# Performance work log

Hardware: AMD Instinct MI355X
Metric: run time of the kernel (lower is better)

The kernel has to match this reference:

```python
import jax, jax.numpy as jnp
import numpy as np

N, E, F_IN = 50000, 800000, 64
H, C1, C2 = 4, 32, 64
NUM_GRAPHS, NUM_CLASSES = 128, 8
NEG_SLOPE = 0.2


def _glorot(key, shape):
    fan_in, fan_out = shape[1], shape[0]
    lim = (6.0 / (fan_in + fan_out)) ** 0.5
    return jax.random.uniform(key, shape, jnp.float32, -lim, lim)


def setup_inputs() -> dict:
    key = jax.random.key(0)
    ks = jax.random.split(key, 20)
    x = jax.random.normal(ks[0], (N, F_IN), jnp.float32)
    edge_index = jax.random.randint(ks[1], (2, E), 0, N, jnp.int64)
    batch = jnp.sort(jax.random.randint(ks[2], (N,), 0, NUM_GRAPHS, jnp.int64))
    d1, d2 = H * C1, H * C2
    return {
        "x": x, "edge_index": edge_index, "batch": batch,
        # GATv2 layer 1 (F_IN -> 32, 4 heads)
        "Wl1": _glorot(ks[3], (d1, F_IN)), "bl1": jnp.zeros((d1,), jnp.float32),
        "Wr1": _glorot(ks[4], (d1, F_IN)), "br1": jnp.zeros((d1,), jnp.float32),
        "att1": _glorot(ks[5], (H, C1)), "bias1": jnp.zeros((d1,), jnp.float32),
        # GATv2 layer 2 (128 -> 64, 4 heads)
        "Wl2": _glorot(ks[6], (d2, d1)), "bl2": jnp.zeros((d2,), jnp.float32),
        "Wr2": _glorot(ks[7], (d2, d1)), "br2": jnp.zeros((d2,), jnp.float32),
        "att2": _glorot(ks[8], (H, C2)), "bias2": jnp.zeros((d2,), jnp.float32),
        # classifier: Linear(256,128) -> ReLU -> (Dropout eval=id) -> Linear(128,8)
        "Wf1": _glorot(ks[9], (128, d2)), "bf1": jnp.zeros((128,), jnp.float32),
        "Wf2": _glorot(ks[10], (NUM_CLASSES, 128)), "bf2": jnp.zeros((NUM_CLASSES,), jnp.float32),
    }


def _gatv2(x, src, dst, Wl, bl, Wr, br, att, bias, heads, out_ch):
    # PyG GATv2Conv: xl = lin_l(x) (source), xr = lin_r(x) (target)
    xl = (x @ Wl.T + bl).reshape(N, heads, out_ch)
    xr = (x @ Wr.T + br).reshape(N, heads, out_ch)
    # per-edge score: att . LeakyReLU(xl[j] + xr[i])  -> [E', H]
    e = jnp.sum(jax.nn.leaky_relu(xl[src] + xr[dst], NEG_SLOPE) * att, axis=-1)
    # destination-grouped softmax (self-loops guarantee every node has an edge)
    emax = jax.ops.segment_max(e, dst, num_segments=N)
    ex = jnp.exp(e - emax[dst])
    denom = jax.ops.segment_sum(ex, dst, num_segments=N)
    alpha = ex / denom[dst]  # [E', H]
    out = jax.ops.segment_sum(alpha[:, :, None] * xl[src], dst, num_segments=N)
    return out.reshape(N, heads * out_ch) + bias


def reference(x, edge_index, batch, Wl1, bl1, Wr1, br1, att1, bias1,
              Wl2, bl2, Wr2, br2, att2, bias2, Wf1, bf1, Wf2, bf2):
    # add self loops (PyG default add_self_loops=True)
    loops = jnp.arange(N, dtype=edge_index.dtype)
    src = jnp.concatenate([edge_index[0], loops])
    dst = jnp.concatenate([edge_index[1], loops])
    h = jax.nn.elu(_gatv2(x, src, dst, Wl1, bl1, Wr1, br1, att1, bias1, H, C1))
    h = jax.nn.elu(_gatv2(h, src, dst, Wl2, bl2, Wr2, br2, att2, bias2, H, C2))
    # global mean pool over graphs
    sums = jax.ops.segment_sum(h, batch, num_segments=NUM_GRAPHS)
    cnts = jax.ops.segment_sum(jnp.ones((N,), h.dtype), batch, num_segments=NUM_GRAPHS)
    pooled = sums / jnp.maximum(cnts, 1.0)[:, None]  # [G, 256]
    # classifier (dropout inactive at inference)
    z = jax.nn.relu(pooled @ Wf1.T + bf1)
    return z @ Wf2.T + bf2
```

## Files before the change

kernel.cpp:

```cpp
#include <hip/hip_runtime.h>
#include <hip/hip_bf16.h>
#include <math.h>

#define NN 50000
#define NE 800000
#define NEP (NE + NN)
#define NG 128
#define PSPLIT 16

typedef unsigned short u16;
typedef __bf16 bf16x8 __attribute__((ext_vector_type(8)));
typedef float f32x4 __attribute__((ext_vector_type(4)));

__device__ __forceinline__ float lrelu02(float v) {
  return fmaxf(v, 0.0f) + 0.2f * fminf(v, 0.0f);
}
__device__ __forceinline__ float eluf(float v) {
  return v > 0.0f ? v : expm1f(v);
}
__device__ __forceinline__ float bflo(unsigned u) {
  union { unsigned i; float f; } c; c.i = u << 16; return c.f;
}
__device__ __forceinline__ float bfhi(unsigned u) {
  union { unsigned i; float f; } c; c.i = u & 0xffff0000u; return c.f;
}
__device__ __forceinline__ bf16x8 load8(const u16* p) {
  union { uint4 u; bf16x8 v; } c;
  c.u = *(const uint4*)p;
  return c.v;
}

__global__ __launch_bounds__(256) void k_deg(const int* __restrict__ ei, int* __restrict__ deg) {
  int t = blockIdx.x * 256 + threadIdx.x;
  if (t >= NEP) return;
  int dst = (t < NE) ? ei[NE + t] : (t - NE);
  atomicAdd(&deg[dst], 1);
}

__global__ __launch_bounds__(1024) void k_scan(const int* __restrict__ deg, int* __restrict__ rowptr) {
  __shared__ int part[1024];
  int t = threadIdx.x;
  const int CH = (NN + 1023) >> 10;
  int b = t * CH;
  int e = min(b + CH, NN);
  int s = 0;
  for (int i = b; i < e; ++i) s += deg[i];
  part[t] = s;
  __syncthreads();
  for (int off = 1; off < 1024; off <<= 1) {
    int v = (t >= off) ? part[t - off] : 0;
    __syncthreads();
    part[t] += v;
    __syncthreads();
  }
  int run = (t == 0) ? 0 : part[t - 1];
  for (int i = b; i < e; ++i) { rowptr[i] = run; run += deg[i]; }
  if (t == 1023) rowptr[NN] = part[1023];
}

__global__ __launch_bounds__(256) void k_scatter(const int* __restrict__ ei, const int* __restrict__ rowptr,
                                                 int* __restrict__ fill, int* __restrict__ srcidx) {
  int t = blockIdx.x * 256 + threadIdx.x;
  if (t >= NEP) return;
  int src, dst;
  if (t < NE) { src = ei[t]; dst = ei[NE + t]; } else { src = t - NE; dst = src; }
  int pos = atomicAdd(&fill[dst], 1);
  srcidx[rowptr[dst] + pos] = src;
}

__global__ __launch_bounds__(256) void k_cvtx(const float* __restrict__ x, u16* __restrict__ o, int n4) {
  int t = blockIdx.x * 256 + threadIdx.x;
  if (t >= n4) return;
  float4 v = ((const float4*)x)[t];
  __hip_bfloat16 b[4] = {__float2bfloat16(v.x), __float2bfloat16(v.y),
                         __float2bfloat16(v.z), __float2bfloat16(v.w)};
  ((uint2*)o)[t] = *(uint2*)b;
}

__global__ __launch_bounds__(256) void k_cvtw(const float* __restrict__ w1, const float* __restrict__ w2,
                                              const float* __restrict__ w3, const float* __restrict__ w4,
                                              u16* __restrict__ o) {
  int t = blockIdx.x * 256 + threadIdx.x;
  if (t >= 81920) return;
  float v;
  if (t < 8192) v = w1[t];
  else if (t < 16384) v = w2[t - 8192];
  else if (t < 49152) v = w3[t - 16384];
  else v = w4[t - 49152];
  __hip_bfloat16 b = __float2bfloat16(v);
  o[t] = *(u16*)&b;
}

template <int K>
__global__ __launch_bounds__(256) void k_mfma(const u16* __restrict__ Xb,
                                              const u16* __restrict__ Wlb, const u16* __restrict__ Wrb,
                                              const float* __restrict__ bl, const float* __restrict__ br,
                                              __hip_bfloat16* __restrict__ Yl, float* __restrict__ Yr,
                                              int dout) {
  int lane = threadIdx.x & 63;
  int wid = threadIdx.x >> 6;
  int r0 = blockIdx.x * 64 + wid * 16;
  int c0 = blockIdx.y * 64;
  bool isR = (blockIdx.z != 0);
  const u16* W = isR ? Wrb : Wlb;
  const float* bias = isR ? br : bl;

  int arow = min(r0 + (lane & 15), NN - 1);
  int koff = (lane >> 4) * 8;
  const u16* ap = Xb + (size_t)arow * K + koff;
  const u16* bp = W + (size_t)(c0 + (lane & 15)) * K + koff;

  f32x4 acc[4] = {};
#pragma unroll
  for (int ks = 0; ks < K / 32; ++ks) {
    bf16x8 a  = load8(ap + ks * 32);
    bf16x8 b0 = load8(bp + ks * 32);
    bf16x8 b1 = load8(bp + 16 * K + ks * 32);
    bf16x8 b2 = load8(bp + 32 * K + ks * 32);
    bf16x8 b3 = load8(bp + 48 * K + ks * 32);
    acc[0] = __builtin_amdgcn_mfma_f32_16x16x32_bf16(a, b0, acc[0], 0, 0, 0);
    acc[1] = __builtin_amdgcn_mfma_f32_16x16x32_bf16(a, b1, acc[1], 0, 0, 0);
    acc[2] = __builtin_amdgcn_mfma_f32_16x16x32_bf16(a, b2, acc[2], 0, 0, 0);
    acc[3] = __builtin_amdgcn_mfma_f32_16x16x32_bf16(a, b3, acc[3], 0, 0, 0);
  }

  int orow = r0 + ((lane >> 4) << 2);
  int ocol = c0 + (lane & 15);
#pragma unroll
  for (int t = 0; t < 4; ++t) {
    int col = ocol + t * 16;
    float bv = bias[col];
    if (!isR) {
#pragma unroll
      for (int v = 0; v < 4; ++v) {
        int row = orow + v;
        if (row < NN) Yl[(size_t)row * dout + col] = __float2bfloat16(acc[t][v] + bv);
      }
    } else {
#pragma unroll
      for (int v = 0; v < 4; ++v) {
        int row = orow + v;
        if (row < NN) Yr[(size_t)row * dout + col] = acc[t][v] + bv;
      }
    }
  }
}

template <int D, bool OBF16>
__global__ __launch_bounds__(256) void k_fused(const int* __restrict__ rowptr, const int* __restrict__ srcidx,
                                               const __hip_bfloat16* __restrict__ xl, const float* __restrict__ xr,
                                               const float* __restrict__ att, const float* __restrict__ bias,
                                               void* __restrict__ outv) {
  constexpr int V = D / 64;
  int lane = threadIdx.x & 63;
  int node = blockIdx.x * 4 + (threadIdx.x >> 6);
  if (node >= NN) return;
  int lo = rowptr[node], hi = rowptr[node + 1];

  float xrv[V], attv[V];
#pragma unroll
  for (int q = 0; q < V; ++q) {
    xrv[q]  = xr[(size_t)node * D + lane * V + q];
    attv[q] = att[lane * V + q];
  }

  const unsigned* xl1 = (const unsigned*)xl;
  const uint2*    xl2 = (const uint2*)xl;

  float denom = 0.f;
  float acc[V] = {};

  auto gather = [&](int j, float* xv) {
    if constexpr (V == 2) {
      unsigned u = xl1[(size_t)j * (D / 2) + lane];
      xv[0] = bflo(u); xv[1] = bfhi(u);
    } else {
      uint2 u = xl2[(size_t)j * (D / 4) + lane];
      xv[0] = bflo(u.x); xv[1] = bfhi(u.x);
      xv[2] = bflo(u.y); xv[3] = bfhi(u.y);
    }
  };
  auto score_partial = [&](const float* xv) {
    float p = 0.f;
#pragma unroll
    for (int q = 0; q < V; ++q) p += attv[q] * lrelu02(xv[q] + xrv[q]);
    return p;
  };
  auto update = [&](float sh, const float* xv) {
    float w = __expf(sh);
    denom += w;
#pragma unroll
    for (int q = 0; q < V; ++q) acc[q] += w * xv[q];
  };

  int s = lo;
  for (; s + 3 < hi; s += 4) {
    int j0 = srcidx[s], j1 = srcidx[s + 1], j2 = srcidx[s + 2], j3 = srcidx[s + 3];
    float xv0[V], xv1[V], xv2[V], xv3[V];
    gather(j0, xv0); gather(j1, xv1); gather(j2, xv2); gather(j3, xv3);
    float p0 = score_partial(xv0);
    float p1 = score_partial(xv1);
    float p2 = score_partial(xv2);
    float p3 = score_partial(xv3);
#pragma unroll
    for (int off = 1; off < 16; off <<= 1) {
      p0 += __shfl_xor(p0, off);
      p1 += __shfl_xor(p1, off);
      p2 += __shfl_xor(p2, off);
      p3 += __shfl_xor(p3, off);
    }
    update(p0, xv0); update(p1, xv1); update(p2, xv2); update(p3, xv3);
  }
  for (; s < hi; ++s) {
    int j0 = srcidx[s];
    float xv0[V];
    gather(j0, xv0);
    float p0 = score_partial(xv0);
#pragma unroll
    for (int off = 1; off < 16; off <<= 1) p0 += __shfl_xor(p0, off);
    update(p0, xv0);
  }

  float rd = 1.0f / denom;
  float vals[V];
#pragma unroll
  for (int q = 0; q < V; ++q) vals[q] = eluf(acc[q] * rd + bias[lane * V + q]);

  if constexpr (OBF16) {
    __hip_bfloat16 tmp[V];
#pragma unroll
    for (int q = 0; q < V; ++q) tmp[q] = __float2bfloat16(vals[q]);
    if constexpr (V == 2) ((unsigned*)outv)[(size_t)node * (D / 2) + lane] = *(unsigned*)tmp;
    else                  ((uint2*)outv)[(size_t)node * (D / 4) + lane] = *(uint2*)tmp;
  } else {
    float* out = (float*)outv;
#pragma unroll
    for (int q = 0; q < V; ++q) out[(size_t)node * D + lane * V + q] = vals[q];
  }
}

__device__ __forceinline__ int lowerb(const int* __restrict__ a, int n, int v) {
  int lo = 0, hi = n;
  while (lo < hi) { int mid = (lo + hi) >> 1; if (a[mid] < v) lo = mid + 1; else hi = mid; }
  return lo;
}

__global__ __launch_bounds__(256) void k_pool(const float* __restrict__ h2, const int* __restrict__ batch,
                                              float* __restrict__ pooled_p) {
  int g = blockIdx.x, sp = blockIdx.y, t = threadIdx.x;
  __shared__ int sh[2];
  if (t < 2) sh[t] = lowerb(batch, NN, g + t);
  __syncthreads();
  int lo = sh[0], hi = sh[1];
  int cnt = hi - lo;
  int chunk = (cnt + PSPLIT - 1) / PSPLIT;
  int b = lo + sp * chunk;
  int e = min(b + chunk, hi);
  float acc = 0.f;
  for (int n = b; n < e; ++n) acc += h2[(size_t)n * 256 + t];
  pooled_p[((size_t)g * PSPLIT + sp) * 256 + t] = acc;
}

__global__ __launch_bounds__(128) void k_cls(const float* __restrict__ pooled_p, const int* __restrict__ batch,
                                             const float* __restrict__ Wf1, const float* __restrict__ bf1,
                                             const float* __restrict__ Wf2, const float* __restrict__ bf2,
                                             float* __restrict__ out) {
  __shared__ float p[256];
  __shared__ float z[128];
  __shared__ int sh[2];
  int g = blockIdx.x, t = threadIdx.x;
  if (t < 2) sh[t] = lowerb(batch, NN, g + t);
  __syncthreads();
  float cnt = (float)(sh[1] - sh[0]);
  float rinv = 1.0f / fmaxf(cnt, 1.0f);
  const float* pp = pooled_p + (size_t)g * PSPLIT * 256;
#pragma unroll 1
  for (int c = t; c < 256; c += 128) {
    float s = 0.f;
#pragma unroll
    for (int sp = 0; sp < PSPLIT; ++sp) s += pp[sp * 256 + c];
    p[c] = s * rinv;
  }
  __syncthreads();
  float a = bf1[t];
  const float* wr = Wf1 + (size_t)t * 256;
  for (int k = 0; k < 256; ++k) a += p[k] * wr[k];
  z[t] = fmaxf(a, 0.f);
  __syncthreads();
  if (t < 8) {
    float o = bf2[t];
    const float* w2 = Wf2 + t * 128;
    for (int k = 0; k < 128; ++k) o += z[k] * w2[k];
    out[g * 8 + t] = o;
  }
}

extern "C" void kernel_launch(void* const* d_in, const int* in_sizes, int n_in,
                              void* d_out, int out_size, void* d_ws, size_t ws_size,
                              hipStream_t stream) {
  const float* x     = (const float*)d_in[0];
  const int*   ei    = (const int*)d_in[1];
  const int*   batch = (const int*)d_in[2];
  const float* Wl1 = (const float*)d_in[3];
  const float* bl1 = (const float*)d_in[4];
  const float* Wr1 = (const float*)d_in[5];
  const float* br1 = (const float*)d_in[6];
  const float* att1  = (const float*)d_in[7];
  const float* bias1 = (const float*)d_in[8];
  const float* Wl2 = (const float*)d_in[9];
  const float* bl2 = (const float*)d_in[10];
  const float* Wr2 = (const float*)d_in[11];
  const float* br2 = (const float*)d_in[12];
  const float* att2  = (const float*)d_in[13];
  const float* bias2 = (const float*)d_in[14];
  const float* Wf1 = (const float*)d_in[15];
  const float* bf1 = (const float*)d_in[16];
  const float* Wf2 = (const float*)d_in[17];
  const float* bf2 = (const float*)d_in[18];
  float* out = (float*)d_out;

  char* w = (char*)d_ws;
  size_t off = 0;
  auto alloc = [&](size_t bytes) -> void* {
    void* p = w + off;
    off += (bytes + 255) & ~(size_t)255;
    return p;
  };
  int* rowptr = (int*)alloc((NN + 1) * sizeof(int));
  int* deg    = (int*)alloc(NN * sizeof(int));
  int* fill   = (int*)alloc(NN * sizeof(int));
  int* srcidx = (int*)alloc((size_t)NEP * sizeof(int));
  u16* Xb1    = (u16*)alloc((size_t)NN * 64 * sizeof(u16));
  u16* Wb     = (u16*)alloc((size_t)81920 * sizeof(u16));
  u16* Wl1b = Wb, *Wr1b = Wb + 8192, *Wl2b = Wb + 16384, *Wr2b = Wb + 49152;
  char* regA  = (char*)alloc((size_t)NN * 128 * 2 + (size_t)NN * 128 * 4);
  __hip_bfloat16* xl1 = (__hip_bfloat16*)regA;
  float*          xr1 = (float*)(regA + (size_t)NN * 128 * 2);
  __hip_bfloat16* xl2 = (__hip_bfloat16*)regA;
  u16*   h1b    = (u16*)alloc((size_t)NN * 128 * sizeof(u16));
  float* xr2    = (float*)alloc((size_t)NN * 256 * sizeof(float));
  float* h2     = xr2;
  float* pooled_p = (float*)alloc((size_t)NG * PSPLIT * 256 * sizeof(float));
  (void)ws_size; (void)in_sizes; (void)n_in; (void)out_size;

  hipMemsetAsync(deg, 0, NN * sizeof(int), stream);
  hipMemsetAsync(fill, 0, NN * sizeof(int), stream);

  const int EB = (NEP + 255) / 256;
  k_deg<<<EB, 256, 0, stream>>>(ei, deg);
  k_scan<<<1, 1024, 0, stream>>>(deg, rowptr);
  k_scatter<<<EB, 256, 0, stream>>>(ei, rowptr, fill, srcidx);

  k_cvtx<<<(NN * 64 / 4 + 255) / 256, 256, 0, stream>>>(x, Xb1, NN * 64 / 4);
  k_cvtw<<<(81920 + 255) / 256, 256, 0, stream>>>(Wl1, Wr1, Wl2, Wr2, Wb);

  const int RB = (NN + 63) / 64;
  dim3 g1(RB, 2, 2);
  k_mfma<64><<<g1, 256, 0, stream>>>(Xb1, Wl1b, Wr1b, bl1, br1, xl1, xr1, 128);
  k_fused<128, true><<<(NN + 3) / 4, 256, 0, stream>>>(rowptr, srcidx, xl1, xr1, att1, bias1, h1b);

  dim3 g2(RB, 4, 2);
  k_mfma<128><<<g2, 256, 0, stream>>>(h1b, Wl2b, Wr2b, bl2, br2, xl2, xr2, 256);
  k_fused<256, false><<<(NN + 3) / 4, 256, 0, stream>>>(rowptr, srcidx, xl2, xr2, att2, bias2, h2);

  dim3 gp(NG, PSPLIT);
  k_pool<<<gp, 256, 0, stream>>>(h2, batch, pooled_p);
  k_cls<<<NG, 128, 0, stream>>>(pooled_p, batch, Wf1, bf1, Wf2, bf2, out);
}
```

Baseline: 421.6 us.

## Decompose leaky-ReLU score into abs plus per-node linear terms, multi-edge gathers

Rewrites LeakyReLU(v) as 0.6v+0.4|v|, so the linear part of each edge score splits into a per-source term, precomputed by a new k_att kernel, and a per-destination term computed once per node. The inner loop then needs only one fma with fabs per element. Weights use exp2 with log2e folded into the scale factors. The gather is also restructured so each lane loads 16 bytes and one wavefront handles several edges at once, with a cross-subgroup shuffle reduction at the end. This adds an extra kernel pass, and the softmax still runs without max subtraction, so very large scores could overflow.

```diff
diff --git a/kernel.cpp b/kernel.cpp
--- a/kernel.cpp
+++ b/kernel.cpp
@@ -12,9 +12,8 @@
 typedef __bf16 bf16x8 __attribute__((ext_vector_type(8)));
 typedef float f32x4 __attribute__((ext_vector_type(4)));
 
-__device__ __forceinline__ float lrelu02(float v) {
-  return fmaxf(v, 0.0f) + 0.2f * fminf(v, 0.0f);
-}
+#define L2E 1.4426950408889634f
+
 __device__ __forceinline__ float eluf(float v) {
   return v > 0.0f ? v : expm1f(v);
 }
@@ -28,6 +27,12 @@
   union { uint4 u; bf16x8 v; } c;
   c.u = *(const uint4*)p;
   return c.v;
+}
+__device__ __forceinline__ void unpack8(uint4 u, float* xv) {
+  xv[0] = bflo(u.x); xv[1] = bfhi(u.x);
+  xv[2] = bflo(u.y); xv[3] = bfhi(u.y);
+  xv[4] = bflo(u.z); xv[5] = bfhi(u.z);
+  xv[6] = bflo(u.w); xv[7] = bfhi(u.w);
 }
 
 __global__ __launch_bounds__(256) void k_deg(const int* __restrict__ ei, int* __restrict__ deg) {
@@ -146,96 +151,123 @@
   }
 }
 
-template <int D, bool OBF16>
+template <int C>
+__global__ __launch_bounds__(256) void k_att(const u16* __restrict__ xl, const float* __restrict__ att,
+                                             float* __restrict__ Alp) {
+  constexpr int D = 4 * C, LPE = D / 8, EPW = 64 / LPE, HL = C / 8;
+  int lane = threadIdx.x & 63;
+  int il = lane % LPE, sub = lane / LPE;
+  int node = blockIdx.x * (4 * EPW) + (threadIdx.x >> 6) * EPW + sub;
+  if (node >= NN) return;
+  uint4 u = ((const uint4*)xl)[(size_t)node * (D / 8) + il];
+  float xv[8];
+  unpack8(u, xv);
+  float p = 0.f;
+#pragma unroll
+  for (int q = 0; q < 8; ++q) p = fmaf(att[il * 8 + q], xv[q], p);
+#pragma unroll
+  for (int off = 1; off < HL; off <<= 1) p += __shfl_xor(p, off);
+  if ((il % HL) == 0) Alp[node * 4 + il / HL] = p * (0.6f * L2E);
+}
+
+template <int C, bool OBF16>
 __global__ __launch_bounds__(256) void k_fused(const int* __restrict__ rowptr, const int* __restrict__ srcidx,
-                                               const __hip_bfloat16* __restrict__ xl, const float* __restrict__ xr,
-                                               const float* __restrict__ att, const float* __restrict__ bias,
-                                               void* __restrict__ outv) {
-  constexpr int V = D / 64;
+                                               const u16* __restrict__ xl, const float* __restrict__ xr,
+                                               const float* __restrict__ Alp, const float* __restrict__ att,
+                                               const float* __restrict__ bias, void* __restrict__ outv) {
+  constexpr int D = 4 * C, LPE = D / 8, EPW = 64 / LPE, HL = C / 8;
   int lane = threadIdx.x & 63;
   int node = blockIdx.x * 4 + (threadIdx.x >> 6);
   if (node >= NN) return;
+  int il = lane % LPE, sub = lane / LPE;
+  int h = il / HL;
   int lo = rowptr[node], hi = rowptr[node + 1];
 
-  float xrv[V], attv[V];
-#pragma unroll
-  for (int q = 0; q < V; ++q) {
-    xrv[q]  = xr[(size_t)node * D + lane * V + q];
-    attv[q] = att[lane * V + q];
-  }
-
-  const unsigned* xl1 = (const unsigned*)xl;
-  const uint2*    xl2 = (const uint2*)xl;
-
+  float xrv[8], attv[8];
+  float rpart = 0.f;
+#pragma unroll
+  for (int q = 0; q < 8; ++q) {
+    float a = att[il * 8 + q] * (0.4f * L2E);
+    float v = xr[(size_t)node * D + il * 8 + q];
+    attv[q] = a; xrv[q] = v;
+    rpart = fmaf(a, v, rpart);
+  }
+#pragma unroll
+  for (int off = 1; off < HL; off <<= 1) rpart += __shfl_xor(rpart, off);
+  rpart *= 1.5f;
+
+  const uint4* xt = (const uint4*)xl;
   float denom = 0.f;
-  float acc[V] = {};
-
-  auto gather = [&](int j, float* xv) {
-    if constexpr (V == 2) {
-      unsigned u = xl1[(size_t)j * (D / 2) + lane];
-      xv[0] = bflo(u); xv[1] = bfhi(u);
-    } else {
-      uint2 u = xl2[(size_t)j * (D / 4) + lane];
-      xv[0] = bflo(u.x); xv[1] = bfhi(u.x);
-      xv[2] = bflo(u.y); xv[3] = bfhi(u.y);
+  float acc[8] = {};
+
+  int s0 = lo;
+  for (; s0 + 2 * EPW <= hi; s0 += 2 * EPW) {
+    int j0 = srcidx[s0 + sub];
+    int j1 = srcidx[s0 + EPW + sub];
+    uint4 u0 = xt[(size_t)j0 * (D / 8) + il];
+    uint4 u1 = xt[(size_t)j1 * (D / 8) + il];
+    float a0 = Alp[j0 * 4 + h], a1 = Alp[j1 * 4 + h];
+    float xv0[8], xv1[8];
+    unpack8(u0, xv0); unpack8(u1, xv1);
+    float p0 = 0.f, p1 = 0.f;
+#pragma unroll
+    for (int q = 0; q < 8; ++q) {
+      p0 = fmaf(attv[q], fabsf(xv0[q] + xrv[q]), p0);
+      p1 = fmaf(attv[q], fabsf(xv1[q] + xrv[q]), p1);
     }
-  };
-  auto score_partial = [&](const float* xv) {
-    float p = 0.f;
-#pragma unroll
-    for (int q = 0; q < V; ++q) p += attv[q] * lrelu02(xv[q] + xrv[q]);
-    return p;
-  };
-  auto update = [&](float sh, const float* xv) {
-    float w = __expf(sh);
-    denom += w;
-#pragma unroll
-    for (int q = 0; q < V; ++q) acc[q] += w * xv[q];
-  };
-
-  int s = lo;
-  for (; s + 3 < hi; s += 4) {
-    int j0 = srcidx[s], j1 = srcidx[s + 1], j2 = srcidx[s + 2], j3 = srcidx[s + 3];
-    float xv0[V], xv1[V], xv2[V], xv3[V];
-    gather(j0, xv0); gather(j1, xv1); gather(j2, xv2); gather(j3, xv3);
-    float p0 = score_partial(xv0);
-    float p1 = score_partial(xv1);
-    float p2 = score_partial(xv2);
-    float p3 = score_partial(xv3);
-#pragma unroll
-    for (int off = 1; off < 16; off <<= 1) {
+#pragma unroll
+    for (int off = 1; off < HL; off <<= 1) {
       p0 += __shfl_xor(p0, off);
       p1 += __shfl_xor(p1, off);
-      p2 += __shfl_xor(p2, off);
-      p3 += __shfl_xor(p3, off);
     }
-    update(p0, xv0); update(p1, xv1); update(p2, xv2); update(p3, xv3);
-  }
-  for (; s < hi; ++s) {
-    int j0 = srcidx[s];
-    float xv0[V];
-    gather(j0, xv0);
-    float p0 = score_partial(xv0);
-#pragma unroll
-    for (int off = 1; off < 16; off <<= 1) p0 += __shfl_xor(p0, off);
-    update(p0, xv0);
-  }
-
-  float rd = 1.0f / denom;
-  float vals[V];
-#pragma unroll
-  for (int q = 0; q < V; ++q) vals[q] = eluf(acc[q] * rd + bias[lane * V + q]);
-
-  if constexpr (OBF16) {
-    __hip_bfloat16 tmp[V];
-#pragma unroll
-    for (int q = 0; q < V; ++q) tmp[q] = __float2bfloat16(vals[q]);
-    if constexpr (V == 2) ((unsigned*)outv)[(size_t)node * (D / 2) + lane] = *(unsigned*)tmp;
-    else                  ((uint2*)outv)[(size_t)node * (D / 4) + lane] = *(uint2*)tmp;
-  } else {
-    float* out = (float*)outv;
-#pragma unroll
-    for (int q = 0; q < V; ++q) out[(size_t)node * D + lane * V + q] = vals[q];
+    float w0 = exp2f(p0 + rpart + a0);
+    float w1 = exp2f(p1 + rpart + a1);
+    denom += w0 + w1;
+#pragma unroll
+    for (int q = 0; q < 8; ++q) acc[q] = fmaf(w1, xv1[q], fmaf(w0, xv0[q], acc[q]));
+  }
+  for (; s0 < hi; s0 += EPW) {
+    int e = s0 + sub;
+    bool valid = e < hi;
+    int j = srcidx[valid ? e : lo];
+    uint4 u = xt[(size_t)j * (D / 8) + il];
+    float al = Alp[j * 4 + h];
+    float xv[8];
+    unpack8(u, xv);
+    float p = 0.f;
+#pragma unroll
+    for (int q = 0; q < 8; ++q) p = fmaf(attv[q], fabsf(xv[q] + xrv[q]), p);
+#pragma unroll
+    for (int off = 1; off < HL; off <<= 1) p += __shfl_xor(p, off);
+    float w = valid ? exp2f(p + rpart + al) : 0.f;
+    denom += w;
+#pragma unroll
+    for (int q = 0; q < 8; ++q) acc[q] = fmaf(w, xv[q], acc[q]);
+  }
+
+#pragma unroll
+  for (int off = LPE; off < 64; off <<= 1) {
+    denom += __shfl_xor(denom, off);
+#pragma unroll
+    for (int q = 0; q < 8; ++q) acc[q] += __shfl_xor(acc[q], off);
+  }
+
+  if (sub == 0) {
+    float rd = 1.0f / denom;
+    float vals[8];
+#pragma unroll
+    for (int q = 0; q < 8; ++q) vals[q] = eluf(fmaf(acc[q], rd, bias[il * 8 + q]));
+    if constexpr (OBF16) {
+      __hip_bfloat16 tmp[8];
+#pragma unroll
+      for (int q = 0; q < 8; ++q) tmp[q] = __float2bfloat16(vals[q]);
+      ((uint4*)outv)[(size_t)node * (D / 8) + il] = *(uint4*)tmp;
+    } else {
+      float4 f0 = {vals[0], vals[1], vals[2], vals[3]};
+      float4 f1 = {vals[4], vals[5], vals[6], vals[7]};
+      ((float4*)outv)[(size_t)node * (D / 4) + il * 2]     = f0;
+      ((float4*)outv)[(size_t)node * (D / 4) + il * 2 + 1] = f1;
+    }
   }
 }
 
@@ -341,6 +373,8 @@
   float* xr2    = (float*)alloc((size_t)NN * 256 * sizeof(float));
   float* h2     = xr2;
   float* pooled_p = (float*)alloc((size_t)NG * PSPLIT * 256 * sizeof(float));
+  float* Al1p   = (float*)alloc((size_t)NN * 4 * sizeof(float));
+  float* Al2p   = (float*)alloc((size_t)NN * 4 * sizeof(float));
   (void)ws_size; (void)in_sizes; (void)n_in; (void)out_size;
 
   hipMemsetAsync(deg, 0, NN * sizeof(int), stream);
@@ -357,11 +391,15 @@
   const int RB = (NN + 63) / 64;
   dim3 g1(RB, 2, 2);
   k_mfma<64><<<g1, 256, 0, stream>>>(Xb1, Wl1b, Wr1b, bl1, br1, xl1, xr1, 128);
-  k_fused<128, true><<<(NN + 3) / 4, 256, 0, stream>>>(rowptr, srcidx, xl1, xr1, att1, bias1, h1b);
+  k_att<32><<<(NN + 15) / 16, 256, 0, stream>>>((const u16*)xl1, att1, Al1p);
+  k_fused<32, true><<<(NN + 3) / 4, 256, 0, stream>>>(rowptr, srcidx, (const u16*)xl1, xr1,
+                                                      Al1p, att1, bias1, h1b);
 
   dim3 g2(RB, 4, 2);
   k_mfma<128><<<g2, 256, 0, stream>>>(h1b, Wl2b, Wr2b, bl2, br2, xl2, xr2, 256);
-  k_fused<256, false><<<(NN + 3) / 4, 256, 0, stream>>>(rowptr, srcidx, xl2, xr2, att2, bias2, h2);
+  k_att<64><<<(NN + 7) / 8, 256, 0, stream>>>((const u16*)xl2, att2, Al2p);
+  k_fused<64, false><<<(NN + 3) / 4, 256, 0, stream>>>(rowptr, srcidx, (const u16*)xl2, xr2,
+                                                       Al2p, att2, bias2, h2);
 
   dim3 gp(NG, PSPLIT);
   k_pool<<<gp, 256, 0, stream>>>(h2, batch, pooled_p);
```

Measured after the change: 444.6 us. 5.5% more time.
